# Optimization experiments

Measured on AMD Instinct MI355X. Metric: run time of the kernel, lower is better.

## Reference

```python
import jax, jax.numpy as jnp
import numpy as np

B, L, D = 2, 2048, 2048
H, KVH, HD, FD = 8, 1, 256, 64   # heads, kv heads, head_dim, feature_dim
CHUNK = 64


def setup_inputs() -> dict:
    key = jax.random.key(0)
    ks = jax.random.split(key, 8)
    hidden_states = jax.random.normal(ks[0], (B, L, D), dtype=jnp.float32)
    # Gemma-style RoPE tables over half the head dim
    half = HD // 2
    inv_freq = 1.0 / (10000.0 ** (jnp.arange(half, dtype=jnp.float32) / half))
    ang = jnp.arange(L, dtype=jnp.float32)[:, None] * inv_freq[None, :]  # [L, half]
    freqs_cos, freqs_sin = jnp.cos(ang), jnp.sin(ang)
    mask = jnp.ones((1, 1, L, L), dtype=bool)  # unused in linear path
    s = 0.02
    Wq = jax.random.normal(ks[1], (D, H * HD), dtype=jnp.float32) * s
    Wk = jax.random.normal(ks[2], (D, KVH * HD), dtype=jnp.float32) * s
    Wv = jax.random.normal(ks[3], (D, KVH * HD), dtype=jnp.float32) * s
    Wo = jax.random.normal(ks[4], (H * HD, D), dtype=jnp.float32) * s
    fmq = jax.random.normal(ks[5], (H, HD, FD), dtype=jnp.float32) * s
    fmk = jax.random.normal(ks[6], (H, HD, FD), dtype=jnp.float32) * s
    return dict(hidden_states=hidden_states, freqs_cos=freqs_cos, freqs_sin=freqs_sin,
                mask=mask, Wq=Wq, Wk=Wk, Wv=Wv, Wo=Wo, fmq=fmq, fmk=fmk)


def _rope(x, cos, sin):
    # x: [B, L, h, HD]; Gemma complex RoPE: first half = real, second half = imag
    half = x.shape[-1] // 2
    x1, x2 = x[..., :half], x[..., half:]
    c = cos[None, :, None, :]
    s = sin[None, :, None, :]
    return jnp.concatenate([x1 * c - x2 * s, x1 * s + x2 * c], axis=-1)


def _hedgehog(x, W):
    # x: [B, H, L, HD], W: [H, HD, FD] -> softmax over cat([xW, -xW]) -> [B,H,L,2*FD]
    p = jnp.einsum('bhld,hdf->bhlf', x, W)
    return jax.nn.softmax(jnp.concatenate([p, -p], axis=-1), axis=-1)


def _chunk_linear_attn(q, k, v, chunk=CHUNK):
    # q,k: [B,H,L,F]; v: [B,H,L,HD]; chunked causal linear attention
    b, h, l, f = q.shape
    dv = v.shape[-1]
    n = l // chunk
    q = q.reshape(b, h, n, chunk, f) * (f ** -0.5)
    k = k.reshape(b, h, n, chunk, f)
    v = v.reshape(b, h, n, chunk, dv)
    kv = jnp.einsum('bhncf,bhncd->bhnfd', k, v)            # per-chunk KV
    kv = jnp.cumsum(kv, axis=2)
    kv = jnp.concatenate([jnp.zeros_like(kv[:, :, :1]), kv[:, :, :-1]], axis=2)  # exclusive prefix
    inter = jnp.einsum('bhncf,bhnfd->bhncd', q, kv)        # cross-chunk term
    s = jnp.einsum('bhnif,bhnjf->bhnij', q, k)             # intra-chunk scores
    tri = jnp.tril(jnp.ones((chunk, chunk), dtype=bool))
    s = jnp.where(tri, s, 0.0)
    intra = jnp.einsum('bhnij,bhnjd->bhnid', s, v)
    return (inter + intra).reshape(b, h, l, dv)


def reference(hidden_states, freqs_cos, freqs_sin, mask, Wq, Wk, Wv, Wo, fmq, fmk):
    b, l, _ = hidden_states.shape
    q = (hidden_states @ Wq).reshape(b, l, H, HD)
    k = (hidden_states @ Wk).reshape(b, l, KVH, HD)
    v = (hidden_states @ Wv).reshape(b, l, KVH, HD)
    q = _rope(q, freqs_cos, freqs_sin)
    k = _rope(k, freqs_cos, freqs_sin)
    # repeat_interleave kv heads to num_heads (MQA expansion)
    rep = H // KVH
    k = jnp.repeat(k, rep, axis=2)
    v = jnp.repeat(v, rep, axis=2)
    q = jnp.transpose(q, (0, 2, 1, 3))  # [B,H,L,HD]
    k = jnp.transpose(k, (0, 2, 1, 3))
    v = jnp.transpose(v, (0, 2, 1, 3))
    q = _hedgehog(q, fmq)
    k = _hedgehog(k, fmk)
    o = _chunk_linear_attn(q, k, v)                         # [B,H,L,HD]
    o = jnp.transpose(o, (0, 2, 1, 3)).reshape(b, l, H * HD)
    return o @ Wo
```

## Files before the change

### kernel.cpp

```cpp
#include <hip/hip_runtime.h>

#define B_ 2
#define L_ 2048
#define D_ 2048
#define H_ 8
#define HD_ 256
#define FD_ 64
#define F_ 128
#define NC_ 32
#define M_ (B_*L_)
#define SCALE_Q 0.08838834764831845f

typedef unsigned short u16;
typedef __attribute__((ext_vector_type(8))) short bf16x8;
typedef __attribute__((ext_vector_type(8))) unsigned short u16x8;
typedef __attribute__((ext_vector_type(16))) float f32x16;
typedef __attribute__((ext_vector_type(4))) unsigned int u32x4;

#define FMA4(a_, s_, v_) { (a_).x += (s_)*(v_).x; (a_).y += (s_)*(v_).y; \
                           (a_).z += (s_)*(v_).z; (a_).w += (s_)*(v_).w; }


__device__ __forceinline__ u16 bf16_rne(float x) {
  unsigned u = __float_as_uint(x);
  return (u16)((u + 0x7fffu + ((u >> 16) & 1u)) >> 16);
}
__device__ __forceinline__ void bf16_split(float x, u16& h, u16& l) {
  unsigned u = __float_as_uint(x);
  unsigned hb = (u + 0x7fffu + ((u >> 16) & 1u)) >> 16;
  h = (u16)hb;
  float hf = __uint_as_float(hb << 16);
  l = bf16_rne(x - hf);
}

__device__ __forceinline__ void gl_lds16(const u16* g, u16* l) {
  __builtin_amdgcn_global_load_lds(
      (const __attribute__((address_space(1))) unsigned int*)g,
      (__attribute__((address_space(3))) unsigned int*)l, 16, 0, 0);
}

__device__ __forceinline__ size_t kvb_off(int d, int f) {
  return (size_t)(((d >> 7) & 1) * 16384 + ((f >> 5) & 3) * 4096 +
                  ((d >> 6) & 1) * 2048 + ((f >> 4) & 1) * 1024 +
                  ((d >> 5) & 1) * 512 + ((f >> 3) & 1) * 256 +
                  (d & 31) * 8 + (f & 7));
}
__device__ __forceinline__ size_t vb_off(int d, int j) {
  return (size_t)(((d >> 7) & 1) * 8192 + ((j >> 5) & 1) * 4096 +
                  ((d >> 6) & 1) * 2048 + ((j >> 4) & 1) * 1024 +
                  ((d >> 5) & 1) * 512 + ((j >> 3) & 1) * 256 +
                  (d & 31) * 8 + (j & 7));
}

__device__ __forceinline__ void wtrans_body(const float* __restrict__ W, int Nsrc,
                                            int n0, u16* __restrict__ dst,
                                            int P, int kt) {
  int t = threadIdx.x;
  int nn = t & 127, kh = t >> 7;
  const float* src = W + (size_t)(kt * 32 + kh * 16) * Nsrc + n0 + nn;
  u16x8 u0, u1;
  #pragma unroll
  for (int kk = 0; kk < 8; ++kk) u0[kk] = bf16_rne(src[(size_t)kk * Nsrc]);
  #pragma unroll
  for (int kk = 0; kk < 8; ++kk) u1[kk] = bf16_rne(src[(size_t)(kk + 8) * Nsrc]);
  size_t base = ((size_t)P * 64 + kt) * 4096 + (size_t)((nn >> 6) & 1) * 2048
              + (size_t)kh * 1024 + (size_t)((nn >> 5) & 1) * 512
              + (size_t)(nn & 31) * 8;
  *(u16x8*)(dst + base) = u0;
  *(u16x8*)(dst + base + 256) = u1;
}

__global__ __launch_bounds__(256)
void prep_kernel(const float* __restrict__ hs,
                 const float* __restrict__ Wq, const float* __restrict__ Wk,
                 const float* __restrict__ Wv,
                 u16* __restrict__ hsHt, u16* __restrict__ hsLt,
                 u16* __restrict__ WTh) {
  int bid = blockIdx.x;
  if (bid < 4096) {
    int gid = bid * 256 + threadIdx.x;
    int r = gid >> 8, u = gid & 255;
    const float* src = hs + (size_t)r * 2048 + u * 8;
    float4 v0 = *(const float4*)src, v1 = *(const float4*)(src + 4);
    float vals[8] = {v0.x, v0.y, v0.z, v0.w, v1.x, v1.y, v1.z, v1.w};
    u16x8 hv, lv;
    #pragma unroll
    for (int j = 0; j < 8; ++j) { u16 hh, ll; bf16_split(vals[j], hh, ll); hv[j] = hh; lv[j] = ll; }
    size_t off = ((size_t)(r >> 6) * 64 + (u >> 2)) * 2048
               + (size_t)((u >> 1) & 1) * 1024 + (size_t)((r >> 5) & 1) * 512
               + (size_t)(u & 1) * 256 + (size_t)(r & 31) * 8;
    *(u16x8*)(hsHt + off) = hv;
    *(u16x8*)(hsLt + off) = lv;
  } else {
    int idx = bid - 4096;
    int P = idx >> 6, kt = idx & 63;
    const float* W; int Nsrc, n0;
    if (P < 16)      { W = Wq; Nsrc = 2048; n0 = P * 128; }
    else if (P < 18) { W = Wk; Nsrc = 256;  n0 = (P - 16) * 128; }
    else             { W = Wv; Nsrc = 256;  n0 = (P - 18) * 128; }
    wtrans_body(W, Nsrc, n0, WTh, P, kt);
  }
}

__global__ __launch_bounds__(256)
void prep_o(const float* __restrict__ o, u16* __restrict__ oHt,
            u16* __restrict__ oLt) {
  int gid = blockIdx.x * 256 + threadIdx.x;
  int r = gid >> 8, u = gid & 255;
  const float* src = o + (size_t)r * 2048 + u * 8;
  float4 v0 = *(const float4*)src, v1 = *(const float4*)(src + 4);
  float vals[8] = {v0.x, v0.y, v0.z, v0.w, v1.x, v1.y, v1.z, v1.w};
  u16x8 hv, lv;
  #pragma unroll
  for (int j = 0; j < 8; ++j) { u16 hh, ll; bf16_split(vals[j], hh, ll); hv[j] = hh; lv[j] = ll; }
  size_t off = ((size_t)(r >> 6) * 64 + (u >> 2)) * 2048
             + (size_t)((u >> 1) & 1) * 1024 + (size_t)((r >> 5) & 1) * 512
             + (size_t)(u & 1) * 256 + (size_t)(r & 31) * 8;
  *(u16x8*)(oHt + off) = hv;
  *(u16x8*)(oLt + off) = lv;
}

__global__ __launch_bounds__(256)
void prep_v(const float* __restrict__ v, u16* __restrict__ vbH,
            u16* __restrict__ vbL) {
  int bn = blockIdx.x;
  const float* vp = v + (size_t)bn * 64 * HD_;
  size_t cbout = (size_t)bn * 16384;
  int d = threadIdx.x;
  #pragma unroll
  for (int it = 0; it < 8; ++it) {
    int j0 = it * 8;
    u16x8 hv, lv;
    #pragma unroll
    for (int c = 0; c < 8; ++c) {
      u16 hh, ll; bf16_split(vp[(size_t)(j0 + c) * HD_ + d], hh, ll);
      hv[c] = hh; lv[c] = ll;
    }
    size_t off = cbout + vb_off(d, j0);
    *(u16x8*)(vbH + off) = hv;
    *(u16x8*)(vbL + off) = lv;
  }
}

__global__ __launch_bounds__(256)
void wtrans_wo(const float* __restrict__ Wo, u16* __restrict__ WoTh) {
  wtrans_body(Wo, 2048, blockIdx.x * 128, WoTh, blockIdx.x, blockIdx.y);
}

__device__ __forceinline__ void mfma_body(
    const u16* __restrict__ AtH, const u16* __restrict__ AtL,
    const u16* __restrict__ Bt, float* __restrict__ C, int cstride,
    int bm, int bn) {
  __shared__ __align__(16) u16 AsH[2048];
  __shared__ __align__(16) u16 AsL[2048];
  __shared__ __align__(16) u16 Bs[4096];
  const int t = threadIdx.x, lane = t & 63, wv = t >> 6;
  const u16* aSrc = (wv ? AtL : AtH) + (size_t)bm * 131072 + lane * 8;
  const u16* bSrc = Bt + (size_t)bn * 262144 + wv * 2048 + lane * 8;
  u16* aDst = wv ? AsL : AsH;
  u16* bDst = Bs + wv * 2048;

  f32x16 acc[2][2];
  #pragma unroll
  for (int a = 0; a < 2; ++a)
    #pragma unroll
    for (int b2 = 0; b2 < 2; ++b2)
      #pragma unroll
      for (int r = 0; r < 16; ++r) acc[a][b2][r] = 0.f;

  for (int kt = 0; kt < 64; ++kt) {
    const u16* ak = aSrc + (size_t)kt * 2048;
    const u16* bk = bSrc + (size_t)kt * 4096;
    __syncthreads();
    #pragma unroll
    for (int c = 0; c < 4; ++c) {
      gl_lds16(ak + c * 512, aDst + c * 512);
      gl_lds16(bk + c * 512, bDst + c * 512);
    }
    __syncthreads();

    #pragma unroll
    for (int ks = 0; ks < 2; ++ks) {
      const u16* ph = AsH + ks * 1024 + lane * 8;
      const u16* pl = AsL + ks * 1024 + lane * 8;
      const u16* pb = Bs + wv * 2048 + ks * 1024 + lane * 8;
      bf16x8 a0 = *(const bf16x8*)ph;
      bf16x8 a1 = *(const bf16x8*)(ph + 512);
      bf16x8 b0 = *(const bf16x8*)pb;
      bf16x8 b1 = *(const bf16x8*)(pb + 512);
      acc[0][0] = __builtin_amdgcn_mfma_f32_32x32x16_bf16(a0, b0, acc[0][0], 0, 0, 0);
      acc[0][1] = __builtin_amdgcn_mfma_f32_32x32x16_bf16(a0, b1, acc[0][1], 0, 0, 0);
      acc[1][0] = __builtin_amdgcn_mfma_f32_32x32x16_bf16(a1, b0, acc[1][0], 0, 0, 0);
      acc[1][1] = __builtin_amdgcn_mfma_f32_32x32x16_bf16(a1, b1, acc[1][1], 0, 0, 0);
      bf16x8 l0 = *(const bf16x8*)pl;
      bf16x8 l1 = *(const bf16x8*)(pl + 512);
      acc[0][0] = __builtin_amdgcn_mfma_f32_32x32x16_bf16(l0, b0, acc[0][0], 0, 0, 0);
      acc[0][1] = __builtin_amdgcn_mfma_f32_32x32x16_bf16(l0, b1, acc[0][1], 0, 0, 0);
      acc[1][0] = __builtin_amdgcn_mfma_f32_32x32x16_bf16(l1, b0, acc[1][0], 0, 0, 0);
      acc[1][1] = __builtin_amdgcn_mfma_f32_32x32x16_bf16(l1, b1, acc[1][1], 0, 0, 0);
    }
  }

  const int fr = lane & 31, g = lane >> 5;
  float* Cp = C + (size_t)(bm * 64) * cstride + wv * 64;
  #pragma unroll
  for (int mt = 0; mt < 2; ++mt)
    #pragma unroll
    for (int nt = 0; nt < 2; ++nt) {
      #pragma unroll
      for (int r = 0; r < 16; ++r) {
        int row = mt * 32 + (r & 3) + 8 * (r >> 2) + 4 * g;
        Cp[(size_t)row * cstride + nt * 32 + fr] = acc[mt][nt][r];
      }
    }
}

#define SUB_ 20480
#define MFB(a_, b_, c_) (c_) = __builtin_amdgcn_mfma_f32_32x32x16_bf16((a_), (b_), (c_), 0, 0, 0)

__device__ __forceinline__ void mfma_big_body(
    const u16* __restrict__ AtH, const u16* __restrict__ AtL,
    const u16* __restrict__ Bt, float* __restrict__ C, int cstride,
    int bm, int bn) {
  __shared__ __align__(16) u16 lds[3 * SUB_];
  const int t = threadIdx.x, lane = t & 63, wv = t >> 6;
  const int wm = wv >> 1, wn = wv & 1;

  const u16* gs[5];
  unsigned lo[5], gst[5];
  #pragma unroll
  for (int j = 0; j < 5; ++j) {
    int line = wv * 5 + j;
    if (line < 16) {
      gs[j] = AtH + ((size_t)(4 * bm + (line >> 2)) * 64) * 2048
                  + (size_t)(line & 3) * 512 + lane * 8;
      lo[j] = line * 512; gst[j] = 2048;
    } else if (line < 32) {
      int l2 = line - 16;
      gs[j] = AtL + ((size_t)(4 * bm + (l2 >> 2)) * 64) * 2048
                  + (size_t)(l2 & 3) * 512 + lane * 8;
      lo[j] = 8192 + l2 * 512; gst[j] = 2048;
    } else {
      int l3 = line - 32;
      gs[j] = Bt + (size_t)bn * 262144 + (size_t)l3 * 512 + lane * 8;
      lo[j] = 16384 + l3 * 512; gst[j] = 4096;
    }
  }

  f32x16 acc[2][2];
  #pragma unroll
  for (int a = 0; a < 2; ++a)
    #pragma unroll
    for (int b2 = 0; b2 < 2; ++b2)
      #pragma unroll
      for (int r = 0; r < 16; ++r) acc[a][b2][r] = 0.f;

  #pragma unroll
  for (int j = 0; j < 5; ++j) gl_lds16(gs[j], lds + lo[j]);
  #pragma unroll
  for (int j = 0; j < 5; ++j) gl_lds16(gs[j] + gst[j], lds + SUB_ + lo[j]);
  asm volatile("s_waitcnt vmcnt(5)" ::: "memory");
  __builtin_amdgcn_s_barrier();
  __builtin_amdgcn_sched_barrier(0);

  int cb = 0;
  for (int kt = 0; kt < 64; ++kt) {
    int sb = cb + 2 * SUB_; if (sb >= 3 * SUB_) sb -= 3 * SUB_;
    const u16* base = lds + cb;
    const u16* ph0 = base + wm * 2048 + lane * 8;
    const u16* pb0 = base + 16384 + wn * 2048 + lane * 8;

    bf16x8 a0 = *(const bf16x8*)(ph0);
    bf16x8 a1 = *(const bf16x8*)(ph0 + 512);
    bf16x8 l0 = *(const bf16x8*)(ph0 + 8192);
    bf16x8 l1 = *(const bf16x8*)(ph0 + 8704);
    bf16x8 b0 = *(const bf16x8*)(pb0);
    bf16x8 b1 = *(const bf16x8*)(pb0 + 512);
    if (kt < 62) {
      gl_lds16(gs[0] + (size_t)(kt + 2) * gst[0], lds + sb + lo[0]);
      gl_lds16(gs[1] + (size_t)(kt + 2) * gst[1], lds + sb + lo[1]);
      gl_lds16(gs[2] + (size_t)(kt + 2) * gst[2], lds + sb + lo[2]);
    }
    __builtin_amdgcn_s_barrier();
    asm volatile("s_waitcnt lgkmcnt(0)" ::: "memory");
    __builtin_amdgcn_sched_barrier(0);
    __builtin_amdgcn_s_setprio(1);
    MFB(a0, b0, acc[0][0]); MFB(a0, b1, acc[0][1]);
    MFB(a1, b0, acc[1][0]); MFB(a1, b1, acc[1][1]);
    MFB(l0, b0, acc[0][0]); MFB(l0, b1, acc[0][1]);
    MFB(l1, b0, acc[1][0]); MFB(l1, b1, acc[1][1]);
    __builtin_amdgcn_s_setprio(0);
    __builtin_amdgcn_s_barrier();
    __builtin_amdgcn_sched_barrier(0);

    bf16x8 c0 = *(const bf16x8*)(ph0 + 1024);
    bf16x8 c1 = *(const bf16x8*)(ph0 + 1536);
    bf16x8 m0 = *(const bf16x8*)(ph0 + 9216);
    bf16x8 m1 = *(const bf16x8*)(ph0 + 9728);
    bf16x8 d0 = *(const bf16x8*)(pb0 + 1024);
    bf16x8 d1 = *(const bf16x8*)(pb0 + 1536);
    if (kt < 62) {
      gl_lds16(gs[3] + (size_t)(kt + 2) * gst[3], lds + sb + lo[3]);
      gl_lds16(gs[4] + (size_t)(kt + 2) * gst[4], lds + sb + lo[4]);
    }
    __builtin_amdgcn_s_barrier();
    asm volatile("s_waitcnt lgkmcnt(0)" ::: "memory");
    __builtin_amdgcn_sched_barrier(0);
    __builtin_amdgcn_s_setprio(1);
    MFB(c0, d0, acc[0][0]); MFB(c0, d1, acc[0][1]);
    MFB(c1, d0, acc[1][0]); MFB(c1, d1, acc[1][1]);
    MFB(m0, d0, acc[0][0]); MFB(m0, d1, acc[0][1]);
    MFB(m1, d0, acc[1][0]); MFB(m1, d1, acc[1][1]);
    __builtin_amdgcn_s_setprio(0);
    if (kt < 62) asm volatile("s_waitcnt vmcnt(5)" ::: "memory");
    else         asm volatile("s_waitcnt vmcnt(0)" ::: "memory");
    __builtin_amdgcn_s_barrier();
    __builtin_amdgcn_sched_barrier(0);
    cb += SUB_; if (cb == 3 * SUB_) cb = 0;
  }

  const int fr = lane & 31, g = lane >> 5;
  float* Cp = C + (size_t)(bm * 256 + wm * 64) * cstride + wn * 64;
  #pragma unroll
  for (int mt = 0; mt < 2; ++mt)
    #pragma unroll
    for (int nt = 0; nt < 2; ++nt) {
      #pragma unroll
      for (int r = 0; r < 16; ++r) {
        int row = mt * 32 + (r & 3) + 8 * (r >> 2) + 4 * g;
        Cp[(size_t)row * cstride + nt * 32 + fr] = acc[mt][nt][r];
      }
    }
}

__global__ __launch_bounds__(512, 2)
void mfma_q(const u16* __restrict__ hsHt, const u16* __restrict__ hsLt,
            const u16* __restrict__ WTh, float* __restrict__ q) {
  mfma_big_body(hsHt, hsLt, WTh, q + blockIdx.x * 128, 2048,
                blockIdx.y, blockIdx.x);
}

__global__ __launch_bounds__(128, 4)
void mfma_kv(const u16* __restrict__ hsHt, const u16* __restrict__ hsLt,
             const u16* __restrict__ WTh,
             float* __restrict__ k, float* __restrict__ v) {
  int bn = blockIdx.x;
  float* Cb; int co;
  if (bn < 2) { Cb = k; co = bn * 128; }
  else        { Cb = v; co = (bn - 2) * 128; }
  mfma_body(hsHt, hsLt, WTh, Cb + co, 256, blockIdx.y, 16 + bn);
}

__global__ __launch_bounds__(512, 2)
void mfma_wo(const u16* __restrict__ oHt, const u16* __restrict__ oLt,
             const u16* __restrict__ WoTh, float* __restrict__ out) {
  mfma_big_body(oHt, oLt, WoTh, out + blockIdx.x * 128, 2048,
                blockIdx.y, blockIdx.x);
}

__device__ __forceinline__ float wave_max64(float v) {
  #pragma unroll
  for (int off = 32; off > 0; off >>= 1) v = fmaxf(v, __shfl_xor(v, off, 64));
  return v;
}
__device__ __forceinline__ float wave_sum64(float v) {
  #pragma unroll
  for (int off = 32; off > 0; off >>= 1) v += __shfl_xor(v, off, 64);
  return v;
}

__global__ __launch_bounds__(256)
void hedgehog_kernel(const float* __restrict__ q, const float* __restrict__ kx,
                     const float* __restrict__ fmq, const float* __restrict__ fmk,
                     const float* __restrict__ cosb, const float* __restrict__ sinb,
                     float* __restrict__ qf, float* __restrict__ kf) {
  __shared__ __align__(16) float rows[4][4][256];
  int bid = blockIdx.x;
  const float* x; const float* fm; float* out; int nh_in, gb;
  if (bid < 2048) { x = q;  fm = fmq; out = qf; nh_in = 8; gb = bid * 4; }
  else            { x = kx; fm = fmk; out = kf; nh_in = 1; gb = (bid - 2048) * 4; }
  int wave = threadIdx.x >> 6, lane = threadIdx.x & 63;
  int g = gb + wave;
  int l4 = g & (L_/4 - 1);
  int bh = g / (L_/4);
  int h = bh & 7, b = bh >> 3;
  int l0 = l4 * 4;
  size_t rstride = (nh_in == 1) ? (size_t)HD_ : (size_t)H_ * HD_;
  const float* xrow = (nh_in == 1)
      ? x + (size_t)(b * L_ + l0) * HD_
      : x + ((size_t)(b * L_ + l0) * H_ + h) * HD_;
  int dd = (lane & 31) * 4;
  #pragma unroll
  for (int r = 0; r < 4; ++r) {
    float4 v = *(const float4*)(xrow + r * rstride + lane * 4);
    float4 u;
    u.x = __shfl_xor(v.x, 32, 64); u.y = __shfl_xor(v.y, 32, 64);
    u.z = __shfl_xor(v.z, 32, 64); u.w = __shfl_xor(v.w, 32, 64);
    int l = l0 + r;
    float4 c = *(const float4*)(cosb + (size_t)l * 128 + dd);
    float4 s = *(const float4*)(sinb + (size_t)l * 128 + dd);
    float4 ro;
    if (lane < 32) {
      ro.x = v.x * c.x - u.x * s.x; ro.y = v.y * c.y - u.y * s.y;
      ro.z = v.z * c.z - u.z * s.z; ro.w = v.w * c.w - u.w * s.w;
    } else {
      ro.x = u.x * s.x + v.x * c.x; ro.y = u.y * s.y + v.y * c.y;
      ro.z = u.z * s.z + v.z * c.z; ro.w = u.w * s.w + v.w * c.w;
    }
    *(float4*)&rows[wave][r][lane * 4] = ro;
  }
  __syncthreads();

  const float* fmh = fm + (size_t)h * HD_ * FD_;
  float p0 = 0.f, p1 = 0.f, p2 = 0.f, p3 = 0.f;
  for (int d2 = 0; d2 < HD_; d2 += 4) {
    float w0 = fmh[(d2 + 0) * FD_ + lane];
    float w1 = fmh[(d2 + 1) * FD_ + lane];
    float w2 = fmh[(d2 + 2) * FD_ + lane];
    float w3 = fmh[(d2 + 3) * FD_ + lane];
    float4 r0 = *(const float4*)&rows[wave][0][d2];
    float4 r1 = *(const float4*)&rows[wave][1][d2];
    float4 r2 = *(const float4*)&rows[wave][2][d2];
    float4 r3 = *(const float4*)&rows[wave][3][d2];
    p0 += r0.x * w0 + r0.y * w1 + r0.z * w2 + r0.w * w3;
    p1 += r1.x * w0 + r1.y * w1 + r1.z * w2 + r1.w * w3;
    p2 += r2.x * w0 + r2.y * w1 + r2.z * w2 + r2.w * w3;
    p3 += r3.x * w0 + r3.y * w1 + r3.z * w2 + r3.w * w3;
  }
  float p[4] = {p0, p1, p2, p3};
  #pragma unroll
  for (int r = 0; r < 4; ++r) {
    float m = wave_max64(fabsf(p[r]));
    float e1 = __expf(p[r] - m);
    float e2 = __expf(-p[r] - m);
    float z = wave_sum64(e1 + e2);
    float inv = 1.0f / z;
    size_t base = ((size_t)bh * L_ + l0 + r) * F_;
    out[base + lane]      = e1 * inv;
    out[base + 64 + lane] = e2 * inv;
  }
}

__global__ __launch_bounds__(256)
void chunk_kv_kernel(const float* __restrict__ kf, const float* __restrict__ v,
                     u16* __restrict__ kvbH, u16* __restrict__ kvbL) {
  __shared__ __align__(16) float kfs[64][128];
  int n = blockIdx.x & (NC_ - 1), bh = blockIdx.x >> 5;
  int b = bh >> 3;
  const float* kfp = kf + ((size_t)bh * L_ + (size_t)n * 64) * F_;
  int t = threadIdx.x;
  #pragma unroll
  for (int it = 0; it < 8; ++it) {
    int flat = t * 4 + it * 1024;
    *(float4*)&kfs[flat >> 7][flat & 127] = *(const float4*)(kfp + flat);
  }
  __syncthreads();
  int dg = t & 63;
  int fg = t >> 6;
  const float* vp = v + (size_t)(b * L_ + n * 64) * HD_ + dg * 4;
  size_t cb = (size_t)blockIdx.x * 32768;
  #pragma unroll
  for (int pass = 0; pass < 4; ++pass) {
    int f0 = fg * 8 + pass * 32;
    float4 acc[8];
    #pragma unroll
    for (int i = 0; i < 8; ++i) acc[i] = make_float4(0.f, 0.f, 0.f, 0.f);
    for (int j = 0; j < 64; ++j) {
      float4 vv = *(const float4*)(vp + (size_t)j * HD_);
      float4 ka = *(const float4*)&kfs[j][f0];
      float4 kb = *(const float4*)&kfs[j][f0 + 4];
      FMA4(acc[0], ka.x, vv); FMA4(acc[1], ka.y, vv);
      FMA4(acc[2], ka.z, vv); FMA4(acc[3], ka.w, vv);
      FMA4(acc[4], kb.x, vv); FMA4(acc[5], kb.y, vv);
      FMA4(acc[6], kb.z, vv); FMA4(acc[7], kb.w, vv);
    }
    #pragma unroll
    for (int c = 0; c < 4; ++c) {
      u16x8 hv, lv;
      #pragma unroll
      for (int ff = 0; ff < 8; ++ff) {
        float xs = (c == 0) ? acc[ff].x : (c == 1) ? acc[ff].y
                 : (c == 2) ? acc[ff].z : acc[ff].w;
        u16 hh, ll; bf16_split(xs, hh, ll); hv[ff] = hh; lv[ff] = ll;
      }
      int d = dg * 4 + c;
      size_t off = cb + kvb_off(d, f0);
      *(u16x8*)(kvbH + off) = hv;
      *(u16x8*)(kvbL + off) = lv;
    }
  }
}

__global__ __launch_bounds__(256)
void chunk_scan_kernel(u16* __restrict__ kvbH, u16* __restrict__ kvbL) {
  int bh = blockIdx.x >> 4, g = blockIdx.x & 15;
  int d = threadIdx.x;
  size_t off = kvb_off(d, g * 8);
  float run[8] = {0.f, 0.f, 0.f, 0.f, 0.f, 0.f, 0.f, 0.f};
  for (int n = 0; n < NC_; ++n) {
    size_t a = ((size_t)(bh * 32 + n)) * 32768 + off;
    u16x8 hv = *(u16x8*)(kvbH + a);
    u16x8 lv = *(u16x8*)(kvbL + a);
    u16x8 oh, ol;
    #pragma unroll
    for (int c = 0; c < 8; ++c) {
      float val = __uint_as_float((unsigned)hv[c] << 16)
                + __uint_as_float((unsigned)lv[c] << 16);
      u16 hh, ll; bf16_split(run[c], hh, ll); oh[c] = hh; ol[c] = ll;
      run[c] += val;
    }
    *(u16x8*)(kvbH + a) = oh;
    *(u16x8*)(kvbL + a) = ol;
  }
}

__global__ __launch_bounds__(256, 2)
void chunk_attn_kernel(const float* __restrict__ qf, const float* __restrict__ kf,
                       const u16* __restrict__ vbH, const u16* __restrict__ vbL,
                       const u16* __restrict__ kvbH, const u16* __restrict__ kvbL,
                       float* __restrict__ o) {
  __shared__ __align__(16) u16 lds[32768];
  const int n = blockIdx.x & (NC_ - 1), bh = blockIdx.x >> 5;
  const int h = bh & 7, b = bh >> 3;
  const int t = threadIdx.x;
  const int w = t >> 6, i31 = t & 31, G = (t >> 5) & 1;
  const int l8 = (t & 63) * 8;

  {
    const float* qp = qf + ((size_t)bh * L_ + (size_t)n * 64) * F_;
    const float* kp = kf + ((size_t)bh * L_ + (size_t)n * 64) * F_;
    int o8 = t & 15, ib = t >> 4;
    #pragma unroll
    for (int iter = 0; iter < 4; ++iter) {
      int i = ib + iter * 16;
      int it = i >> 5, ks = o8 >> 1;
      int sub = (it * 8 + ks) * 512 + (o8 & 1) * 256 + (i & 31) * 8;
      {
        const float* src = qp + (size_t)i * 128 + o8 * 8;
        float4 a = *(const float4*)src, c = *(const float4*)(src + 4);
        float vals[8] = {a.x, a.y, a.z, a.w, c.x, c.y, c.z, c.w};
        u16x8 hv, lv;
        #pragma unroll
        for (int j = 0; j < 8; ++j) {
          u16 hh, ll; bf16_split(vals[j] * SCALE_Q, hh, ll);
          hv[j] = hh; lv[j] = ll;
        }
        *(u16x8*)(lds + sub) = hv;
        *(u16x8*)(lds + 8192 + sub) = lv;
      }
      {
        const float* src = kp + (size_t)i * 128 + o8 * 8;
        float4 a = *(const float4*)src, c = *(const float4*)(src + 4);
        float vals[8] = {a.x, a.y, a.z, a.w, c.x, c.y, c.z, c.w};
        u16x8 hv, lv;
        #pragma unroll
        for (int j = 0; j < 8; ++j) {
          u16 hh, ll; bf16_split(vals[j], hh, ll);
          hv[j] = hh; lv[j] = ll;
        }
        *(u16x8*)(lds + 16384 + sub) = hv;
        *(u16x8*)(lds + 24576 + sub) = lv;
      }
    }
  }
  __syncthreads();

  const u16* Lq  = lds;
  const u16* Lql = lds + 8192;
  const u16* Lk  = lds + 16384;
  const u16* Lkl = lds + 24576;

  f32x16 st[2][2];
  #pragma unroll
  for (int a = 0; a < 2; ++a)
    #pragma unroll
    for (int c = 0; c < 2; ++c)
      #pragma unroll
      for (int r = 0; r < 16; ++r) st[a][c][r] = 0.f;

  #pragma unroll
  for (int ks = 0; ks < 8; ++ks) {
    bf16x8 kh0 = *(const bf16x8*)(Lk  + ks * 512 + l8);
    bf16x8 kh1 = *(const bf16x8*)(Lk  + (8 + ks) * 512 + l8);
    bf16x8 kl0 = *(const bf16x8*)(Lkl + ks * 512 + l8);
    bf16x8 kl1 = *(const bf16x8*)(Lkl + (8 + ks) * 512 + l8);
    bf16x8 qh0 = *(const bf16x8*)(Lq  + ks * 512 + l8);
    bf16x8 qh1 = *(const bf16x8*)(Lq  + (8 + ks) * 512 + l8);
    bf16x8 ql0 = *(const bf16x8*)(Lql + ks * 512 + l8);
    bf16x8 ql1 = *(const bf16x8*)(Lql + (8 + ks) * 512 + l8);
    MFB(kh0, qh0, st[0][0]); MFB(kh0, ql0, st[0][0]); MFB(kl0, qh0, st[0][0]);
    MFB(kh0, qh1, st[0][1]); MFB(kh0, ql1, st[0][1]); MFB(kl0, qh1, st[0][1]);
    MFB(kh1, qh0, st[1][0]); MFB(kh1, ql0, st[1][0]); MFB(kl1, qh0, st[1][0]);
    MFB(kh1, qh1, st[1][1]); MFB(kh1, ql1, st[1][1]); MFB(kl1, qh1, st[1][1]);
  }

  bf16x8 sfH[2][4], sfL[2][4];
  #pragma unroll
  for (int mt = 0; mt < 2; ++mt) {
    int iv = mt * 32 + i31;
    #pragma unroll
    for (int ksj = 0; ksj < 4; ++ksj) {
      const int jt = ksj >> 1, kb = ksj & 1;
      unsigned ph[4], pl[4];
      #pragma unroll
      for (int half = 0; half < 2; ++half) {
        u16 hh[4], ll[4];
        #pragma unroll
        for (int c = 0; c < 4; ++c) {
          int r = 8 * kb + 4 * half + c;
          int jv = jt * 32 + (r & 3) + 8 * (r >> 2) + 4 * G;
          float mv = (jv <= iv) ? st[jt][mt][r] : 0.f;
          u16 h_, l_; bf16_split(mv, h_, l_);
          hh[c] = h_; ll[c] = l_;
        }
        ph[half * 2 + 0] = (unsigned)hh[0] | ((unsigned)hh[1] << 16);
        ph[half * 2 + 1] = (unsigned)hh[2] | ((unsigned)hh[3] << 16);
        pl[half * 2 + 0] = (unsigned)ll[0] | ((unsigned)ll[1] << 16);
        pl[half * 2 + 1] = (unsigned)ll[2] | ((unsigned)ll[3] << 16);
      }
      unsigned rH1 = (unsigned)__shfl_xor((int)(G ? ph[0] : ph[2]), 32, 64);
      unsigned rH2 = (unsigned)__shfl_xor((int)(G ? ph[1] : ph[3]), 32, 64);
      unsigned rL1 = (unsigned)__shfl_xor((int)(G ? pl[0] : pl[2]), 32, 64);
      unsigned rL2 = (unsigned)__shfl_xor((int)(G ? pl[1] : pl[3]), 32, 64);
      u32x4 wH, wL;
      wH[0] = G ? rH1 : ph[0]; wH[1] = G ? rH2 : ph[1];
      wH[2] = G ? ph[2] : rH1; wH[3] = G ? ph[3] : rH2;
      wL[0] = G ? rL1 : pl[0]; wL[1] = G ? rL2 : pl[1];
      wL[2] = G ? pl[2] : rL1; wL[3] = G ? pl[3] : rL2;
      sfH[mt][ksj] = __builtin_bit_cast(bf16x8, wH);
      sfL[mt][ksj] = __builtin_bit_cast(bf16x8, wL);
    }
  }

  f32x16 acc[2][2];
  #pragma unroll
  for (int a = 0; a < 2; ++a)
    #pragma unroll
    for (int c = 0; c < 2; ++c)
      #pragma unroll
      for (int r = 0; r < 16; ++r) acc[a][c][r] = 0.f;

  {
    size_t vcb = ((size_t)(b * NC_ + n)) * 16384;
    #pragma unroll
    for (int nt = 0; nt < 2; ++nt) {
      #pragma unroll
      for (int ksj = 0; ksj < 4; ++ksj) {
        size_t basev = vcb + vb_off(w * 64 + nt * 32, ksj * 16) + l8;
        bf16x8 vH = *(const bf16x8*)((const short*)(vbH + basev));
        bf16x8 vL = *(const bf16x8*)((const short*)(vbL + basev));
        MFB(sfH[0][ksj], vH, acc[0][nt]); MFB(sfL[0][ksj], vH, acc[0][nt]);
        MFB(sfH[0][ksj], vL, acc[0][nt]);
        MFB(sfH[1][ksj], vH, acc[1][nt]); MFB(sfL[1][ksj], vH, acc[1][nt]);
        MFB(sfH[1][ksj], vL, acc[1][nt]);
      }
    }
  }

  {
    size_t cb = (size_t)blockIdx.x * 32768;
    #pragma unroll
    for (int ks = 0; ks < 8; ++ks) {
      bf16x8 qa_h0 = *(const bf16x8*)(Lq  + ks * 512 + l8);
      bf16x8 qa_h1 = *(const bf16x8*)(Lq  + (8 + ks) * 512 + l8);
      bf16x8 qa_l0 = *(const bf16x8*)(Lql + ks * 512 + l8);
      bf16x8 qa_l1 = *(const bf16x8*)(Lql + (8 + ks) * 512 + l8);
      #pragma unroll
      for (int nt = 0; nt < 2; ++nt) {
        size_t base = cb + kvb_off(w * 64 + nt * 32, ks * 16) + l8;
        bf16x8 kvH = *(const bf16x8*)((const short*)(kvbH + base));
        bf16x8 kvL = *(const bf16x8*)((const short*)(kvbL + base));
        MFB(qa_h0, kvH, acc[0][nt]); MFB(qa_l0, kvH, acc[0][nt]);
        MFB(qa_h0, kvL, acc[0][nt]);
        MFB(qa_h1, kvH, acc[1][nt]); MFB(qa_l1, kvH, acc[1][nt]);
        MFB(qa_h1, kvL, acc[1][nt]);
      }
    }
  }

  float* op = o + ((size_t)(b * L_ + n * 64)) * 2048 + h * 256 + w * 64;
  #pragma unroll
  for (int mt = 0; mt < 2; ++mt)
    #pragma unroll
    for (int nt = 0; nt < 2; ++nt)
      #pragma unroll
      for (int r = 0; r < 16; ++r) {
        int row = mt * 32 + (r & 3) + 8 * (r >> 2) + 4 * G;
        op[(size_t)row * 2048 + nt * 32 + i31] = acc[mt][nt][r];
      }
}

extern "C" void kernel_launch(void* const* d_in, const int* in_sizes, int n_in,
                              void* d_out, int out_size, void* d_ws, size_t ws_size,
                              hipStream_t stream) {
  const float* hs   = (const float*)d_in[0];
  const float* fcos = (const float*)d_in[1];
  const float* fsin = (const float*)d_in[2];
  const float* Wq  = (const float*)d_in[4];
  const float* Wk  = (const float*)d_in[5];
  const float* Wv  = (const float*)d_in[6];
  const float* Wo  = (const float*)d_in[7];
  const float* fmq = (const float*)d_in[8];
  const float* fmk = (const float*)d_in[9];
  float* out = (float*)d_out;

  float* ws = (float*)d_ws;
  float* q  = ws;
  float* k  = q  + (size_t)M_ * 2048;
  float* v  = k  + (size_t)M_ * 256;
  float* qf = v  + (size_t)M_ * 256;
  float* kf = qf + (size_t)B_ * H_ * L_ * F_;
  float* kvr = kf + (size_t)B_ * H_ * L_ * F_;

  u16* hsHt = (u16*)kvr;
  u16* hsLt = hsHt + (size_t)M_ * 2048;
  u16* WTh  = hsLt + (size_t)M_ * 2048;
  u16* kvbH = (u16*)kvr;
  u16* kvbL = kvbH + (size_t)512 * 32768;
  u16* WoTh = (u16*)kvr;
  u16* vbH  = (u16*)k;
  u16* vbL  = vbH + (size_t)64 * 16384;
  float* o  = q;
  u16* oHt  = (u16*)qf;
  u16* oLt  = (u16*)kf;

  prep_kernel<<<4096 + 1280, 256, 0, stream>>>(hs, Wq, Wk, Wv, hsHt, hsLt, WTh);
  mfma_q<<<dim3(16, 16), 512, 0, stream>>>(hsHt, hsLt, WTh, q);
  mfma_kv<<<dim3(4, 64), 128, 0, stream>>>(hsHt, hsLt, WTh, k, v);
  hedgehog_kernel<<<2048 + 2048, 256, 0, stream>>>(q, k, fmq, fmk, fcos, fsin, qf, kf);
  prep_v<<<B_ * NC_, 256, 0, stream>>>(v, vbH, vbL);
  chunk_kv_kernel<<<B_ * H_ * NC_, 256, 0, stream>>>(kf, v, kvbH, kvbL);
  chunk_scan_kernel<<<256, 256, 0, stream>>>(kvbH, kvbL);
  chunk_attn_kernel<<<B_ * H_ * NC_, 256, 0, stream>>>(qf, kf, vbH, vbL, kvbH, kvbL, o);
  prep_o<<<4096, 256, 0, stream>>>(o, oHt, oLt);
  wtrans_wo<<<dim3(16, 64), 256, 0, stream>>>(Wo, WoTh);
  mfma_wo<<<dim3(16, 16), 512, 0, stream>>>(oHt, oLt, WoTh, out);
}
```

Baseline: 537.9 us.

## Fuse output bf16 split into attention epilogue and merge small prep kernels

```diff
diff --git a/kernel.cpp b/kernel.cpp
--- a/kernel.cpp
+++ b/kernel.cpp
@@ -73,9 +73,9 @@
 __global__ __launch_bounds__(256)
 void prep_kernel(const float* __restrict__ hs,
                  const float* __restrict__ Wq, const float* __restrict__ Wk,
-                 const float* __restrict__ Wv,
+                 const float* __restrict__ Wv, const float* __restrict__ Wo,
                  u16* __restrict__ hsHt, u16* __restrict__ hsLt,
-                 u16* __restrict__ WTh) {
+                 u16* __restrict__ WTh, u16* __restrict__ WoTh) {
   int bid = blockIdx.x;
   if (bid < 4096) {
     int gid = bid * 256 + threadIdx.x;
@@ -91,7 +91,7 @@
                + (size_t)(u & 1) * 256 + (size_t)(r & 31) * 8;
     *(u16x8*)(hsHt + off) = hv;
     *(u16x8*)(hsLt + off) = lv;
-  } else {
+  } else if (bid < 5376) {
     int idx = bid - 4096;
     int P = idx >> 6, kt = idx & 63;
     const float* W; int Nsrc, n0;
@@ -99,46 +99,9 @@
     else if (P < 18) { W = Wk; Nsrc = 256;  n0 = (P - 16) * 128; }
     else             { W = Wv; Nsrc = 256;  n0 = (P - 18) * 128; }
     wtrans_body(W, Nsrc, n0, WTh, P, kt);
-  }
-}
-
-__global__ __launch_bounds__(256)
-void prep_o(const float* __restrict__ o, u16* __restrict__ oHt,
-            u16* __restrict__ oLt) {
-  int gid = blockIdx.x * 256 + threadIdx.x;
-  int r = gid >> 8, u = gid & 255;
-  const float* src = o + (size_t)r * 2048 + u * 8;
-  float4 v0 = *(const float4*)src, v1 = *(const float4*)(src + 4);
-  float vals[8] = {v0.x, v0.y, v0.z, v0.w, v1.x, v1.y, v1.z, v1.w};
-  u16x8 hv, lv;
-  #pragma unroll
-  for (int j = 0; j < 8; ++j) { u16 hh, ll; bf16_split(vals[j], hh, ll); hv[j] = hh; lv[j] = ll; }
-  size_t off = ((size_t)(r >> 6) * 64 + (u >> 2)) * 2048
-             + (size_t)((u >> 1) & 1) * 1024 + (size_t)((r >> 5) & 1) * 512
-             + (size_t)(u & 1) * 256 + (size_t)(r & 31) * 8;
-  *(u16x8*)(oHt + off) = hv;
-  *(u16x8*)(oLt + off) = lv;
-}
-
-__global__ __launch_bounds__(256)
-void prep_v(const float* __restrict__ v, u16* __restrict__ vbH,
-            u16* __restrict__ vbL) {
-  int bn = blockIdx.x;
-  const float* vp = v + (size_t)bn * 64 * HD_;
-  size_t cbout = (size_t)bn * 16384;
-  int d = threadIdx.x;
-  #pragma unroll
-  for (int it = 0; it < 8; ++it) {
-    int j0 = it * 8;
-    u16x8 hv, lv;
-    #pragma unroll
-    for (int c = 0; c < 8; ++c) {
-      u16 hh, ll; bf16_split(vp[(size_t)(j0 + c) * HD_ + d], hh, ll);
-      hv[c] = hh; lv[c] = ll;
-    }
-    size_t off = cbout + vb_off(d, j0);
-    *(u16x8*)(vbH + off) = hv;
-    *(u16x8*)(vbL + off) = lv;
+  } else {
+    int idx = bid - 5376;
+    wtrans_body(Wo, 2048, (idx >> 6) * 128, WoTh, idx >> 6, idx & 63);
   }
 }
 
@@ -373,9 +336,31 @@
 void hedgehog_kernel(const float* __restrict__ q, const float* __restrict__ kx,
                      const float* __restrict__ fmq, const float* __restrict__ fmk,
                      const float* __restrict__ cosb, const float* __restrict__ sinb,
-                     float* __restrict__ qf, float* __restrict__ kf) {
+                     float* __restrict__ qf, float* __restrict__ kf,
+                     const float* __restrict__ vsrc,
+                     u16* __restrict__ vbH, u16* __restrict__ vbL) {
+  int bid = blockIdx.x;
+  if (bid >= 4096) {
+    int bn = bid - 4096;
+    const float* vp = vsrc + (size_t)bn * 64 * HD_;
+    size_t cbout = (size_t)bn * 16384;
+    int d = threadIdx.x;
+    #pragma unroll
+    for (int it = 0; it < 8; ++it) {
+      int j0 = it * 8;
+      u16x8 hv, lv;
+      #pragma unroll
+      for (int c = 0; c < 8; ++c) {
+        u16 hh, ll; bf16_split(vp[(size_t)(j0 + c) * HD_ + d], hh, ll);
+        hv[c] = hh; lv[c] = ll;
+      }
+      size_t off = cbout + vb_off(d, j0);
+      *(u16x8*)(vbH + off) = hv;
+      *(u16x8*)(vbL + off) = lv;
+    }
+    return;
+  }
   __shared__ __align__(16) float rows[4][4][256];
-  int bid = blockIdx.x;
   const float* x; const float* fm; float* out; int nh_in, gb;
   if (bid < 2048) { x = q;  fm = fmq; out = qf; nh_in = 8; gb = bid * 4; }
   else            { x = kx; fm = fmk; out = kf; nh_in = 1; gb = (bid - 2048) * 4; }
@@ -518,7 +503,7 @@
 void chunk_attn_kernel(const float* __restrict__ qf, const float* __restrict__ kf,
                        const u16* __restrict__ vbH, const u16* __restrict__ vbL,
                        const u16* __restrict__ kvbH, const u16* __restrict__ kvbL,
-                       float* __restrict__ o) {
+                       u16* __restrict__ oHt, u16* __restrict__ oLt) {
   __shared__ __align__(16) u16 lds[32768];
   const int n = blockIdx.x & (NC_ - 1), bh = blockIdx.x >> 5;
   const int h = bh & 7, b = bh >> 3;
@@ -678,16 +663,25 @@
     }
   }
 
-  float* op = o + ((size_t)(b * L_ + n * 64)) * 2048 + h * 256 + w * 64;
-  #pragma unroll
-  for (int mt = 0; mt < 2; ++mt)
-    #pragma unroll
-    for (int nt = 0; nt < 2; ++nt)
-      #pragma unroll
-      for (int r = 0; r < 16; ++r) {
-        int row = mt * 32 + (r & 3) + 8 * (r >> 2) + 4 * G;
-        op[(size_t)row * 2048 + nt * 32 + i31] = acc[mt][nt][r];
-      }
+  {
+    int p = b * NC_ + n;
+    #pragma unroll
+    for (int mt = 0; mt < 2; ++mt)
+      #pragma unroll
+      for (int nt = 0; nt < 2; ++nt) {
+        int u_ = h * 32 + w * 8 + nt * 4 + (i31 >> 3);
+        size_t ob = ((size_t)p * 64 + (u_ >> 2)) * 2048
+                  + (size_t)((u_ >> 1) & 1) * 1024 + (size_t)mt * 512
+                  + (size_t)(u_ & 1) * 256 + (size_t)(i31 & 7);
+        #pragma unroll
+        for (int r = 0; r < 16; ++r) {
+          int rr = (r & 3) + 8 * (r >> 2) + 4 * G;
+          u16 hh, ll; bf16_split(acc[mt][nt][r], hh, ll);
+          oHt[ob + (size_t)rr * 8] = hh;
+          oLt[ob + (size_t)rr * 8] = ll;
+        }
+      }
+  }
 }
 
 extern "C" void kernel_launch(void* const* d_in, const int* in_sizes, int n_in,
@@ -717,22 +711,26 @@
   u16* WTh  = hsLt + (size_t)M_ * 2048;
   u16* kvbH = (u16*)kvr;
   u16* kvbL = kvbH + (size_t)512 * 32768;
-  u16* WoTh = (u16*)kvr;
   u16* vbH  = (u16*)k;
   u16* vbL  = vbH + (size_t)64 * 16384;
-  float* o  = q;
-  u16* oHt  = (u16*)qf;
-  u16* oLt  = (u16*)kf;
-
-  prep_kernel<<<4096 + 1280, 256, 0, stream>>>(hs, Wq, Wk, Wv, hsHt, hsLt, WTh);
+  u16* oHt  = (u16*)q;
+  u16* oLt  = oHt + (size_t)M_ * 2048;
+
+  const size_t WS_BASE = (size_t)142606336;
+  bool bigws = ws_size >= WS_BASE + (size_t)8388608;
+  u16* WoTh = bigws ? (u16*)((char*)d_ws + WS_BASE) : (u16*)kvr;
+
+  prep_kernel<<<bigws ? 6400 : 5376, 256, 0, stream>>>(
+      hs, Wq, Wk, Wv, Wo, hsHt, hsLt, WTh, WoTh);
   mfma_q<<<dim3(16, 16), 512, 0, stream>>>(hsHt, hsLt, WTh, q);
   mfma_kv<<<dim3(4, 64), 128, 0, stream>>>(hsHt, hsLt, WTh, k, v);
-  hedgehog_kernel<<<2048 + 2048, 256, 0, stream>>>(q, k, fmq, fmk, fcos, fsin, qf, kf);
-  prep_v<<<B_ * NC_, 256, 0, stream>>>(v, vbH, vbL);
+  hedgehog_kernel<<<4096 + 64, 256, 0, stream>>>(q, k, fmq, fmk, fcos, fsin,
+                                                 qf, kf, v, vbH, vbL);
   chunk_kv_kernel<<<B_ * H_ * NC_, 256, 0, stream>>>(kf, v, kvbH, kvbL);
   chunk_scan_kernel<<<256, 256, 0, stream>>>(kvbH, kvbL);
-  chunk_attn_kernel<<<B_ * H_ * NC_, 256, 0, stream>>>(qf, kf, vbH, vbL, kvbH, kvbL, o);
-  prep_o<<<4096, 256, 0, stream>>>(o, oHt, oLt);
-  wtrans_wo<<<dim3(16, 64), 256, 0, stream>>>(Wo, WoTh);
+  chunk_attn_kernel<<<B_ * H_ * NC_, 256, 0, stream>>>(qf, kf, vbH, vbL,
+                                                       kvbH, kvbL, oHt, oLt);
+  if (!bigws)
+    wtrans_wo<<<dim3(16, 64), 256, 0, stream>>>(Wo, WoTh);
   mfma_wo<<<dim3(16, 16), 512, 0, stream>>>(oHt, oLt, WoTh, out);
 }
```

Result: faster. 503.5 us (-6.4%).
